# Kernel tuning notes

Hardware: AMD Instinct MI355X
Metric: run time of the kernel (lower is better)

The kernel has to match this reference:

```python
import jax, jax.numpy as jnp
import numpy as np

N_NODES = 100000
N_EDGES = 1600000


def _graphconv(h, src, dst, norm_src, norm_dst, W, b, n_nodes):
    # DGL GraphConv, norm='both': D_dst^{-1/2} * A * (D_src^{-1/2} * h) @ W + b, then relu
    h = h * norm_src[:, None]
    agg = jax.ops.segment_sum(h[src], dst, num_segments=n_nodes)  # [N, d] SpMM
    rst = agg @ W  # in_feats <= out_feats path: aggregate first, then W
    rst = rst * norm_dst[:, None]
    rst = rst + b
    return jax.nn.relu(rst)


def setup_inputs() -> dict:
    key = jax.random.key(0)
    ks = jax.random.split(key, 12)
    H = 64
    features = jax.random.normal(ks[0], (N_NODES, H), dtype=jnp.float32)
    src = jax.random.randint(ks[1], (N_EDGES,), 0, N_NODES, dtype=jnp.int64 if jax.config.jax_enable_x64 else jnp.int32)
    dst = jax.random.randint(ks[2], (N_EDGES,), 0, N_NODES, dtype=jnp.int64 if jax.config.jax_enable_x64 else jnp.int32)
    sc = 1.0 / np.sqrt(H)
    W1 = jax.random.normal(ks[3], (H, H), dtype=jnp.float32) * sc
    b1 = jnp.zeros((H,), dtype=jnp.float32)
    W2 = jax.random.normal(ks[4], (H, H), dtype=jnp.float32) * sc
    b2 = jnp.zeros((H,), dtype=jnp.float32)
    W3 = jax.random.normal(ks[5], (H, H), dtype=jnp.float32) * sc
    b3 = jnp.zeros((H,), dtype=jnp.float32)
    Wc = jax.random.normal(ks[6], (H, 10), dtype=jnp.float32) * sc
    bc = jnp.zeros((10,), dtype=jnp.float32)
    return {"features": features, "src": src, "dst": dst,
            "W1": W1, "b1": b1, "W2": W2, "b2": b2, "W3": W3, "b3": b3,
            "Wc": Wc, "bc": bc}


def reference(features, src, dst, W1, b1, W2, b2, W3, b3, Wc, bc):
    n = features.shape[0]
    ones = jnp.ones_like(src, dtype=features.dtype)
    deg_out = jax.ops.segment_sum(ones, src, num_segments=n)
    deg_in = jax.ops.segment_sum(ones, dst, num_segments=n)
    norm_src = jnp.clip(deg_out, 1.0) ** -0.5  # allow_zero_in_degree: clamp(min=1)
    norm_dst = jnp.clip(deg_in, 1.0) ** -0.5
    h = features
    for W, b in ((W1, b1), (W2, b2), (W3, b3)):
        # dropout p=0.0 / eval mode -> identity
        h = _graphconv(h, src, dst, norm_src, norm_dst, W, b, n)
    hg = jnp.mean(h, axis=0, keepdims=True)  # AvgPooling over the single graph -> [1, H]
    logits = hg @ Wc + bc  # [1, n_classes]
    return (logits, hg)
```

## Files before the change

kernel.cpp:

```cpp
#include <hip/hip_runtime.h>


__global__ void deg_kernel(const int* __restrict__ src, int* __restrict__ deg_out, int E) {
  int i = blockIdx.x * blockDim.x + threadIdx.x;
  if (i < E) atomicAdd(&deg_out[src[i]], 1);
}

__global__ void norm_kernel(const int* __restrict__ deg_out, float* __restrict__ ns, int N) {
  int i = blockIdx.x * blockDim.x + threadIdx.x;
  if (i < N) ns[i] = rsqrtf((float)max(deg_out[i], 1));
}

__global__ void fill_kernel(const int* __restrict__ src, const int* __restrict__ dst,
                            int* __restrict__ cursor, int* __restrict__ csr_src, int E) {
  int i = blockIdx.x * blockDim.x + threadIdx.x;
  if (i < E) {
    int d = dst[i];
    int p = atomicAdd(&cursor[d], 1);
    if (p < 64) csr_src[(size_t)d * 64 + p] = src[i];
  }
}

__device__ __forceinline__ ushort f32_to_bf16_rtne(float f) {
  uint u = __float_as_uint(f);
  uint r = (u + 0x7FFFu + ((u >> 16) & 1u)) >> 16;
  return (ushort)r;
}

__global__ __launch_bounds__(256) void gemm_scale_kernel(
    const float* __restrict__ h, const float* __restrict__ W,
    const float* __restrict__ ns, ushort* __restrict__ g, int N) {
  int lane = threadIdx.x & 63;
  int wave = (blockIdx.x << 2) + (threadIdx.x >> 6);
  int nwaves = gridDim.x << 2;
  float wcol[64];
#pragma unroll
  for (int k = 0; k < 64; k++) wcol[k] = W[k * 64 + lane];
  for (int n = wave; n < N; n += nwaves) {
    int nu = __builtin_amdgcn_readfirstlane(n);
    const float* __restrict__ hrow = h + (size_t)nu * 64;
    float acc = 0.f;
#pragma unroll
    for (int k = 0; k < 64; k++) acc = fmaf(hrow[k], wcol[k], acc);
    g[(size_t)nu * 64 + lane] = f32_to_bf16_rtne(acc * ns[nu]);
  }
}

__device__ __forceinline__ float bf16_load(const ushort* p) {
  return __uint_as_float((uint)(*p) << 16);
}

__global__ __launch_bounds__(256) void spmm_kernel(
    const ushort* __restrict__ g, const int* __restrict__ cnt,
    const int* __restrict__ csr_src, const float* __restrict__ bias,
    float* __restrict__ h_out, int N) {
  int lane = threadIdx.x & 63;
  int w = (blockIdx.x << 2) + (threadIdx.x >> 6);
  if (w >= N) return;
  int deg = cnt[w];
  const int* __restrict__ row = csr_src + (size_t)w * 64;
  int end = min(deg, 64);
  float scale = rsqrtf((float)max(deg, 1));
  float b = bias[lane];
  float acc = 0.f;
  int e = 0;
  for (; e + 8 <= end; e += 8) {
    int s0 = row[e + 0], s1 = row[e + 1], s2 = row[e + 2], s3 = row[e + 3];
    int s4 = row[e + 4], s5 = row[e + 5], s6 = row[e + 6], s7 = row[e + 7];
    float a0 = bf16_load(g + (size_t)s0 * 64 + lane);
    float a1 = bf16_load(g + (size_t)s1 * 64 + lane);
    float a2 = bf16_load(g + (size_t)s2 * 64 + lane);
    float a3 = bf16_load(g + (size_t)s3 * 64 + lane);
    float a4 = bf16_load(g + (size_t)s4 * 64 + lane);
    float a5 = bf16_load(g + (size_t)s5 * 64 + lane);
    float a6 = bf16_load(g + (size_t)s6 * 64 + lane);
    float a7 = bf16_load(g + (size_t)s7 * 64 + lane);
    acc += ((a0 + a1) + (a2 + a3)) + ((a4 + a5) + (a6 + a7));
  }
  for (; e + 2 <= end; e += 2) {
    int s0 = row[e + 0], s1 = row[e + 1];
    float a0 = bf16_load(g + (size_t)s0 * 64 + lane);
    float a1 = bf16_load(g + (size_t)s1 * 64 + lane);
    acc += a0 + a1;
  }
  if (e < end) acc += bf16_load(g + (size_t)row[e] * 64 + lane);
  float r = acc * scale + b;
  h_out[(size_t)w * 64 + lane] = fmaxf(r, 0.f);
}

__global__ __launch_bounds__(256) void pool_kernel(const float* __restrict__ h3,
                                                   float* __restrict__ pool, int N) {
  int lane = threadIdx.x & 63;
  int wid = threadIdx.x >> 6;
  float s = 0.f;
  for (int n = (blockIdx.x << 2) + wid; n < N; n += (gridDim.x << 2))
    s += h3[(size_t)n * 64 + lane];
  __shared__ float red[4][64];
  red[wid][lane] = s;
  __syncthreads();
  if (wid == 0) {
    float v = red[0][lane] + red[1][lane] + red[2][lane] + red[3][lane];
    atomicAdd(&pool[lane], v);
  }
}

__global__ void final_kernel(const float* __restrict__ pool, const float* __restrict__ Wc,
                             const float* __restrict__ bc, float* __restrict__ out, float invN) {
  int t = threadIdx.x;
  __shared__ float hg[64];
  float m = pool[t] * invN;
  hg[t] = m;
  out[10 + t] = m;
  __syncthreads();
  if (t < 10) {
    float s = bc[t];
#pragma unroll
    for (int k = 0; k < 64; k++) s = fmaf(hg[k], Wc[k * 10 + t], s);
    out[t] = s;
  }
}

extern "C" void kernel_launch(void* const* d_in, const int* in_sizes, int n_in,
                              void* d_out, int out_size, void* d_ws, size_t ws_size,
                              hipStream_t stream) {
  const float* features = (const float*)d_in[0];
  const int* src = (const int*)d_in[1];
  const int* dst = (const int*)d_in[2];
  const float* W1 = (const float*)d_in[3];
  const float* b1 = (const float*)d_in[4];
  const float* W2 = (const float*)d_in[5];
  const float* b2 = (const float*)d_in[6];
  const float* W3 = (const float*)d_in[7];
  const float* b3 = (const float*)d_in[8];
  const float* Wc = (const float*)d_in[9];
  const float* bc = (const float*)d_in[10];
  float* out = (float*)d_out;

  const int N = in_sizes[0] / 64;
  const int E = in_sizes[1];

  char* ws = (char*)d_ws;
  size_t off = 0;
  auto alloc = [&](size_t bytes) {
    void* p = ws + off;
    off = (off + bytes + 255) & ~(size_t)255;
    return p;
  };
  int* deg_out = (int*)alloc((size_t)N * 4);
  int* cursor = (int*)alloc((size_t)N * 4);
  float* pool = (float*)alloc(64 * 4);
  size_t zero_bytes = off;
  float* ns = (float*)alloc((size_t)N * 4);
  int* csr_src = (int*)alloc((size_t)N * 64 * 4);
  ushort* bufG = (ushort*)alloc((size_t)N * 64 * 2);
  float* bufH = (float*)alloc((size_t)N * 64 * 4);

  hipMemsetAsync(d_ws, 0, zero_bytes, stream);

  int eb = (E + 255) / 256;
  int nb = (N + 255) / 256;
  deg_kernel<<<eb, 256, 0, stream>>>(src, deg_out, E);
  norm_kernel<<<nb, 256, 0, stream>>>(deg_out, ns, N);
  fill_kernel<<<eb, 256, 0, stream>>>(src, dst, cursor, csr_src, E);

  int wb = (N + 3) / 4;

  gemm_scale_kernel<<<2048, 256, 0, stream>>>(features, W1, ns, bufG, N);
  spmm_kernel<<<wb, 256, 0, stream>>>(bufG, cursor, csr_src, b1, bufH, N);
  gemm_scale_kernel<<<2048, 256, 0, stream>>>(bufH, W2, ns, bufG, N);
  spmm_kernel<<<wb, 256, 0, stream>>>(bufG, cursor, csr_src, b2, bufH, N);
  gemm_scale_kernel<<<2048, 256, 0, stream>>>(bufH, W3, ns, bufG, N);
  spmm_kernel<<<wb, 256, 0, stream>>>(bufG, cursor, csr_src, b3, bufH, N);

  pool_kernel<<<256, 256, 0, stream>>>(bufH, pool, N);
  final_kernel<<<1, 64, 0, stream>>>(pool, Wc, bc, out, 1.0f / (float)N);
}
```

Measured before the change: 553.5 us.

## Fuse SpMM with next-layer GEMM, merge graph build kernels, fuse final SpMM with pooling

```diff
diff --git a/kernel.cpp b/kernel.cpp
--- a/kernel.cpp
+++ b/kernel.cpp
@@ -1,23 +1,16 @@
 #include <hip/hip_runtime.h>
 
 
-__global__ void deg_kernel(const int* __restrict__ src, int* __restrict__ deg_out, int E) {
-  int i = blockIdx.x * blockDim.x + threadIdx.x;
-  if (i < E) atomicAdd(&deg_out[src[i]], 1);
-}
-
-__global__ void norm_kernel(const int* __restrict__ deg_out, float* __restrict__ ns, int N) {
-  int i = blockIdx.x * blockDim.x + threadIdx.x;
-  if (i < N) ns[i] = rsqrtf((float)max(deg_out[i], 1));
-}
-
-__global__ void fill_kernel(const int* __restrict__ src, const int* __restrict__ dst,
-                            int* __restrict__ cursor, int* __restrict__ csr_src, int E) {
+__global__ void build_kernel(const int* __restrict__ src, const int* __restrict__ dst,
+                             int* __restrict__ deg_out, int* __restrict__ cursor,
+                             int* __restrict__ csr_src, int E) {
   int i = blockIdx.x * blockDim.x + threadIdx.x;
   if (i < E) {
+    int s = src[i];
     int d = dst[i];
+    atomicAdd(&deg_out[s], 1);
     int p = atomicAdd(&cursor[d], 1);
-    if (p < 64) csr_src[(size_t)d * 64 + p] = src[i];
+    if (p < 64) csr_src[(size_t)d * 64 + p] = s;
   }
 }
 
@@ -27,9 +20,13 @@
   return (ushort)r;
 }
 
-__global__ __launch_bounds__(256) void gemm_scale_kernel(
+__device__ __forceinline__ float bf16_load(const ushort* p) {
+  return __uint_as_float((uint)(*p) << 16);
+}
+
+__global__ __launch_bounds__(256) void gemm1_kernel(
     const float* __restrict__ h, const float* __restrict__ W,
-    const float* __restrict__ ns, ushort* __restrict__ g, int N) {
+    const int* __restrict__ deg_out, ushort* __restrict__ g, int N) {
   int lane = threadIdx.x & 63;
   int wave = (blockIdx.x << 2) + (threadIdx.x >> 6);
   int nwaves = gridDim.x << 2;
@@ -42,61 +39,96 @@
     float acc = 0.f;
 #pragma unroll
     for (int k = 0; k < 64; k++) acc = fmaf(hrow[k], wcol[k], acc);
-    g[(size_t)nu * 64 + lane] = f32_to_bf16_rtne(acc * ns[nu]);
+    float nsv = rsqrtf((float)max(deg_out[nu], 1));
+    g[(size_t)nu * 64 + lane] = f32_to_bf16_rtne(acc * nsv);
   }
 }
 
-__device__ __forceinline__ float bf16_load(const ushort* p) {
-  return __uint_as_float((uint)(*p) << 16);
+__global__ __launch_bounds__(256) void spmm_gemm_kernel(
+    const ushort* __restrict__ g_in, const int* __restrict__ cnt,
+    const int* __restrict__ csr_src, const int* __restrict__ deg_out,
+    const float* __restrict__ bias, const float* __restrict__ W,
+    ushort* __restrict__ g_out, int N) {
+  int lane = threadIdx.x & 63;
+  int wave = (blockIdx.x << 2) + (threadIdx.x >> 6);
+  int nwaves = gridDim.x << 2;
+  float wcol[64];
+#pragma unroll
+  for (int k = 0; k < 64; k++) wcol[k] = W[k * 64 + lane];
+  float b = bias[lane];
+  for (int w0 = wave; w0 < N; w0 += nwaves) {
+    int w = __builtin_amdgcn_readfirstlane(w0);
+    int deg = cnt[w];
+    const int* __restrict__ row = csr_src + (size_t)w * 64;
+    int end = min(deg, 64);
+    float acc = 0.f;
+    int e = 0;
+    for (; e + 8 <= end; e += 8) {
+      int s0 = row[e + 0], s1 = row[e + 1], s2 = row[e + 2], s3 = row[e + 3];
+      int s4 = row[e + 4], s5 = row[e + 5], s6 = row[e + 6], s7 = row[e + 7];
+      float a0 = bf16_load(g_in + (size_t)s0 * 64 + lane);
+      float a1 = bf16_load(g_in + (size_t)s1 * 64 + lane);
+      float a2 = bf16_load(g_in + (size_t)s2 * 64 + lane);
+      float a3 = bf16_load(g_in + (size_t)s3 * 64 + lane);
+      float a4 = bf16_load(g_in + (size_t)s4 * 64 + lane);
+      float a5 = bf16_load(g_in + (size_t)s5 * 64 + lane);
+      float a6 = bf16_load(g_in + (size_t)s6 * 64 + lane);
+      float a7 = bf16_load(g_in + (size_t)s7 * 64 + lane);
+      acc += ((a0 + a1) + (a2 + a3)) + ((a4 + a5) + (a6 + a7));
+    }
+    for (; e + 2 <= end; e += 2) {
+      int s0 = row[e + 0], s1 = row[e + 1];
+      acc += bf16_load(g_in + (size_t)s0 * 64 + lane) + bf16_load(g_in + (size_t)s1 * 64 + lane);
+    }
+    if (e < end) acc += bf16_load(g_in + (size_t)row[e] * 64 + lane);
+    float h = fmaxf(acc * rsqrtf((float)max(deg, 1)) + b, 0.f);
+    float o = 0.f;
+#pragma unroll
+    for (int k = 0; k < 64; k++) o = fmaf(__shfl(h, k, 64), wcol[k], o);
+    float nsv = rsqrtf((float)max(deg_out[w], 1));
+    g_out[(size_t)w * 64 + lane] = f32_to_bf16_rtne(o * nsv);
+  }
 }
 
-__global__ __launch_bounds__(256) void spmm_kernel(
-    const ushort* __restrict__ g, const int* __restrict__ cnt,
+__global__ __launch_bounds__(256) void spmm_pool_kernel(
+    const ushort* __restrict__ g_in, const int* __restrict__ cnt,
     const int* __restrict__ csr_src, const float* __restrict__ bias,
-    float* __restrict__ h_out, int N) {
-  int lane = threadIdx.x & 63;
-  int w = (blockIdx.x << 2) + (threadIdx.x >> 6);
-  if (w >= N) return;
-  int deg = cnt[w];
-  const int* __restrict__ row = csr_src + (size_t)w * 64;
-  int end = min(deg, 64);
-  float scale = rsqrtf((float)max(deg, 1));
-  float b = bias[lane];
-  float acc = 0.f;
-  int e = 0;
-  for (; e + 8 <= end; e += 8) {
-    int s0 = row[e + 0], s1 = row[e + 1], s2 = row[e + 2], s3 = row[e + 3];
-    int s4 = row[e + 4], s5 = row[e + 5], s6 = row[e + 6], s7 = row[e + 7];
-    float a0 = bf16_load(g + (size_t)s0 * 64 + lane);
-    float a1 = bf16_load(g + (size_t)s1 * 64 + lane);
-    float a2 = bf16_load(g + (size_t)s2 * 64 + lane);
-    float a3 = bf16_load(g + (size_t)s3 * 64 + lane);
-    float a4 = bf16_load(g + (size_t)s4 * 64 + lane);
-    float a5 = bf16_load(g + (size_t)s5 * 64 + lane);
-    float a6 = bf16_load(g + (size_t)s6 * 64 + lane);
-    float a7 = bf16_load(g + (size_t)s7 * 64 + lane);
-    acc += ((a0 + a1) + (a2 + a3)) + ((a4 + a5) + (a6 + a7));
-  }
-  for (; e + 2 <= end; e += 2) {
-    int s0 = row[e + 0], s1 = row[e + 1];
-    float a0 = bf16_load(g + (size_t)s0 * 64 + lane);
-    float a1 = bf16_load(g + (size_t)s1 * 64 + lane);
-    acc += a0 + a1;
-  }
-  if (e < end) acc += bf16_load(g + (size_t)row[e] * 64 + lane);
-  float r = acc * scale + b;
-  h_out[(size_t)w * 64 + lane] = fmaxf(r, 0.f);
-}
-
-__global__ __launch_bounds__(256) void pool_kernel(const float* __restrict__ h3,
-                                                   float* __restrict__ pool, int N) {
+    float* __restrict__ pool, int N) {
   int lane = threadIdx.x & 63;
   int wid = threadIdx.x >> 6;
-  float s = 0.f;
-  for (int n = (blockIdx.x << 2) + wid; n < N; n += (gridDim.x << 2))
-    s += h3[(size_t)n * 64 + lane];
+  int wave = (blockIdx.x << 2) + wid;
+  int nwaves = gridDim.x << 2;
+  float b = bias[lane];
+  float psum = 0.f;
+  for (int w0 = wave; w0 < N; w0 += nwaves) {
+    int w = __builtin_amdgcn_readfirstlane(w0);
+    int deg = cnt[w];
+    const int* __restrict__ row = csr_src + (size_t)w * 64;
+    int end = min(deg, 64);
+    float acc = 0.f;
+    int e = 0;
+    for (; e + 8 <= end; e += 8) {
+      int s0 = row[e + 0], s1 = row[e + 1], s2 = row[e + 2], s3 = row[e + 3];
+      int s4 = row[e + 4], s5 = row[e + 5], s6 = row[e + 6], s7 = row[e + 7];
+      float a0 = bf16_load(g_in + (size_t)s0 * 64 + lane);
+      float a1 = bf16_load(g_in + (size_t)s1 * 64 + lane);
+      float a2 = bf16_load(g_in + (size_t)s2 * 64 + lane);
+      float a3 = bf16_load(g_in + (size_t)s3 * 64 + lane);
+      float a4 = bf16_load(g_in + (size_t)s4 * 64 + lane);
+      float a5 = bf16_load(g_in + (size_t)s5 * 64 + lane);
+      float a6 = bf16_load(g_in + (size_t)s6 * 64 + lane);
+      float a7 = bf16_load(g_in + (size_t)s7 * 64 + lane);
+      acc += ((a0 + a1) + (a2 + a3)) + ((a4 + a5) + (a6 + a7));
+    }
+    for (; e + 2 <= end; e += 2) {
+      int s0 = row[e + 0], s1 = row[e + 1];
+      acc += bf16_load(g_in + (size_t)s0 * 64 + lane) + bf16_load(g_in + (size_t)s1 * 64 + lane);
+    }
+    if (e < end) acc += bf16_load(g_in + (size_t)row[e] * 64 + lane);
+    psum += fmaxf(acc * rsqrtf((float)max(deg, 1)) + b, 0.f);
+  }
   __shared__ float red[4][64];
-  red[wid][lane] = s;
+  red[wid][lane] = psum;
   __syncthreads();
   if (wid == 0) {
     float v = red[0][lane] + red[1][lane] + red[2][lane] + red[3][lane];
@@ -150,28 +182,18 @@
   int* cursor = (int*)alloc((size_t)N * 4);
   float* pool = (float*)alloc(64 * 4);
   size_t zero_bytes = off;
-  float* ns = (float*)alloc((size_t)N * 4);
   int* csr_src = (int*)alloc((size_t)N * 64 * 4);
-  ushort* bufG = (ushort*)alloc((size_t)N * 64 * 2);
-  float* bufH = (float*)alloc((size_t)N * 64 * 4);
+  ushort* bufG1 = (ushort*)alloc((size_t)N * 64 * 2);
+  ushort* bufG2 = (ushort*)alloc((size_t)N * 64 * 2);
 
   hipMemsetAsync(d_ws, 0, zero_bytes, stream);
 
   int eb = (E + 255) / 256;
-  int nb = (N + 255) / 256;
-  deg_kernel<<<eb, 256, 0, stream>>>(src, deg_out, E);
-  norm_kernel<<<nb, 256, 0, stream>>>(deg_out, ns, N);
-  fill_kernel<<<eb, 256, 0, stream>>>(src, dst, cursor, csr_src, E);
+  build_kernel<<<eb, 256, 0, stream>>>(src, dst, deg_out, cursor, csr_src, E);
 
-  int wb = (N + 3) / 4;
-
-  gemm_scale_kernel<<<2048, 256, 0, stream>>>(features, W1, ns, bufG, N);
-  spmm_kernel<<<wb, 256, 0, stream>>>(bufG, cursor, csr_src, b1, bufH, N);
-  gemm_scale_kernel<<<2048, 256, 0, stream>>>(bufH, W2, ns, bufG, N);
-  spmm_kernel<<<wb, 256, 0, stream>>>(bufG, cursor, csr_src, b2, bufH, N);
-  gemm_scale_kernel<<<2048, 256, 0, stream>>>(bufH, W3, ns, bufG, N);
-  spmm_kernel<<<wb, 256, 0, stream>>>(bufG, cursor, csr_src, b3, bufH, N);
-
-  pool_kernel<<<256, 256, 0, stream>>>(bufH, pool, N);
+  gemm1_kernel<<<2048, 256, 0, stream>>>(features, W1, deg_out, bufG1, N);
+  spmm_gemm_kernel<<<2048, 256, 0, stream>>>(bufG1, cursor, csr_src, deg_out, b1, W2, bufG2, N);
+  spmm_gemm_kernel<<<2048, 256, 0, stream>>>(bufG2, cursor, csr_src, deg_out, b2, W3, bufG1, N);
+  spmm_pool_kernel<<<2048, 256, 0, stream>>>(bufG1, cursor, csr_src, b3, pool, N);
   final_kernel<<<1, 64, 0, stream>>>(pool, Wc, bc, out, 1.0f / (float)N);
 }
```

After: 579.6 us. +4.7%, slower.

## Build CSR via two-pass bucket sort and fuse last SpMM with pooling

Applied to the files above, without the earlier changes.

```diff
diff --git a/kernel.cpp b/kernel.cpp
--- a/kernel.cpp
+++ b/kernel.cpp
@@ -1,24 +1,45 @@
 #include <hip/hip_runtime.h>
 
 
-__global__ void deg_kernel(const int* __restrict__ src, int* __restrict__ deg_out, int E) {
-  int i = blockIdx.x * blockDim.x + threadIdx.x;
-  if (i < E) atomicAdd(&deg_out[src[i]], 1);
-}
-
-__global__ void norm_kernel(const int* __restrict__ deg_out, float* __restrict__ ns, int N) {
-  int i = blockIdx.x * blockDim.x + threadIdx.x;
-  if (i < N) ns[i] = rsqrtf((float)max(deg_out[i], 1));
-}
-
-__global__ void fill_kernel(const int* __restrict__ src, const int* __restrict__ dst,
-                            int* __restrict__ cursor, int* __restrict__ csr_src, int E) {
+#define CAP 1536
+
+__global__ void bucketA_kernel(const int* __restrict__ src, const int* __restrict__ dst,
+                               int* __restrict__ deg_out, int* __restrict__ bcnt,
+                               uint* __restrict__ bbuf, int E) {
   int i = blockIdx.x * blockDim.x + threadIdx.x;
   if (i < E) {
+    int s = src[i];
     int d = dst[i];
-    int p = atomicAdd(&cursor[d], 1);
-    if (p < 64) csr_src[(size_t)d * 64 + p] = src[i];
-  }
+    atomicAdd(&deg_out[s], 1);
+    int b = d >> 6;
+    int pos = atomicAdd(&bcnt[b], 1);
+    if (pos < CAP) bbuf[(size_t)b * CAP + pos] = ((uint)s << 6) | (uint)(d & 63);
+  }
+}
+
+__global__ __launch_bounds__(256) void bucketB_kernel(const uint* __restrict__ bbuf,
+                                                      const int* __restrict__ bcnt,
+                                                      int* __restrict__ csr_src,
+                                                      int* __restrict__ deg_in, int N) {
+  __shared__ uint stage[64 * 64];
+  __shared__ int lcur[64];
+  int b = blockIdx.x;
+  int tid = threadIdx.x;
+  if (tid < 64) lcur[tid] = 0;
+  __syncthreads();
+  int cnt = min(bcnt[b], CAP);
+  const uint* __restrict__ bb = bbuf + (size_t)b * CAP;
+  for (int i = tid; i < cnt; i += 256) {
+    uint e = bb[i];
+    int dl = e & 63;
+    int p = atomicAdd(&lcur[dl], 1);
+    if (p < 64) stage[dl * 64 + p] = e >> 6;
+  }
+  __syncthreads();
+  int* __restrict__ outp = csr_src + (size_t)b * 4096;
+  for (int i = tid; i < 4096; i += 256) outp[i] = (int)stage[i];
+  int node = b * 64 + tid;
+  if (tid < 64 && node < N) deg_in[node] = min(lcur[tid], 64);
 }
 
 __device__ __forceinline__ ushort f32_to_bf16_rtne(float f) {
@@ -27,9 +48,13 @@
   return (ushort)r;
 }
 
+__device__ __forceinline__ float bf16_load(const ushort* p) {
+  return __uint_as_float((uint)(*p) << 16);
+}
+
 __global__ __launch_bounds__(256) void gemm_scale_kernel(
     const float* __restrict__ h, const float* __restrict__ W,
-    const float* __restrict__ ns, ushort* __restrict__ g, int N) {
+    const int* __restrict__ deg_out, ushort* __restrict__ g, int N) {
   int lane = threadIdx.x & 63;
   int wave = (blockIdx.x << 2) + (threadIdx.x >> 6);
   int nwaves = gridDim.x << 2;
@@ -42,61 +67,96 @@
     float acc = 0.f;
 #pragma unroll
     for (int k = 0; k < 64; k++) acc = fmaf(hrow[k], wcol[k], acc);
-    g[(size_t)nu * 64 + lane] = f32_to_bf16_rtne(acc * ns[nu]);
-  }
-}
-
-__device__ __forceinline__ float bf16_load(const ushort* p) {
-  return __uint_as_float((uint)(*p) << 16);
-}
+    float nsv = rsqrtf((float)max(deg_out[nu], 1));
+    g[(size_t)nu * 64 + lane] = f32_to_bf16_rtne(acc * nsv);
+  }
+}
+
+#define GATHER16(base)                                                   \
+  {                                                                      \
+    int s0 = row[e + 0], s1 = row[e + 1], s2 = row[e + 2], s3 = row[e + 3];   \
+    int s4 = row[e + 4], s5 = row[e + 5], s6 = row[e + 6], s7 = row[e + 7];   \
+    int s8 = row[e + 8], s9 = row[e + 9], sa = row[e + 10], sb = row[e + 11]; \
+    int sc = row[e + 12], sd = row[e + 13], se = row[e + 14], sf = row[e + 15];\
+    float a0 = bf16_load(base + (size_t)s0 * 64 + lane);                 \
+    float a1 = bf16_load(base + (size_t)s1 * 64 + lane);                 \
+    float a2 = bf16_load(base + (size_t)s2 * 64 + lane);                 \
+    float a3 = bf16_load(base + (size_t)s3 * 64 + lane);                 \
+    float a4 = bf16_load(base + (size_t)s4 * 64 + lane);                 \
+    float a5 = bf16_load(base + (size_t)s5 * 64 + lane);                 \
+    float a6 = bf16_load(base + (size_t)s6 * 64 + lane);                 \
+    float a7 = bf16_load(base + (size_t)s7 * 64 + lane);                 \
+    float a8 = bf16_load(base + (size_t)s8 * 64 + lane);                 \
+    float a9 = bf16_load(base + (size_t)s9 * 64 + lane);                 \
+    float aa = bf16_load(base + (size_t)sa * 64 + lane);                 \
+    float ab = bf16_load(base + (size_t)sb * 64 + lane);                 \
+    float ac = bf16_load(base + (size_t)sc * 64 + lane);                 \
+    float ad = bf16_load(base + (size_t)sd * 64 + lane);                 \
+    float ae = bf16_load(base + (size_t)se * 64 + lane);                 \
+    float af = bf16_load(base + (size_t)sf * 64 + lane);                 \
+    acc += (((a0 + a1) + (a2 + a3)) + ((a4 + a5) + (a6 + a7))) +         \
+           (((a8 + a9) + (aa + ab)) + ((ac + ad) + (ae + af)));          \
+  }
 
 __global__ __launch_bounds__(256) void spmm_kernel(
     const ushort* __restrict__ g, const int* __restrict__ cnt,
     const int* __restrict__ csr_src, const float* __restrict__ bias,
     float* __restrict__ h_out, int N) {
   int lane = threadIdx.x & 63;
-  int w = (blockIdx.x << 2) + (threadIdx.x >> 6);
-  if (w >= N) return;
+  int w0 = (blockIdx.x << 2) + (threadIdx.x >> 6);
+  if (w0 >= N) return;
+  int w = __builtin_amdgcn_readfirstlane(w0);
   int deg = cnt[w];
   const int* __restrict__ row = csr_src + (size_t)w * 64;
   int end = min(deg, 64);
-  float scale = rsqrtf((float)max(deg, 1));
   float b = bias[lane];
   float acc = 0.f;
   int e = 0;
-  for (; e + 8 <= end; e += 8) {
+  for (; e + 16 <= end; e += 16) GATHER16(g)
+  for (; e + 4 <= end; e += 4) {
     int s0 = row[e + 0], s1 = row[e + 1], s2 = row[e + 2], s3 = row[e + 3];
-    int s4 = row[e + 4], s5 = row[e + 5], s6 = row[e + 6], s7 = row[e + 7];
     float a0 = bf16_load(g + (size_t)s0 * 64 + lane);
     float a1 = bf16_load(g + (size_t)s1 * 64 + lane);
     float a2 = bf16_load(g + (size_t)s2 * 64 + lane);
     float a3 = bf16_load(g + (size_t)s3 * 64 + lane);
-    float a4 = bf16_load(g + (size_t)s4 * 64 + lane);
-    float a5 = bf16_load(g + (size_t)s5 * 64 + lane);
-    float a6 = bf16_load(g + (size_t)s6 * 64 + lane);
-    float a7 = bf16_load(g + (size_t)s7 * 64 + lane);
-    acc += ((a0 + a1) + (a2 + a3)) + ((a4 + a5) + (a6 + a7));
-  }
-  for (; e + 2 <= end; e += 2) {
-    int s0 = row[e + 0], s1 = row[e + 1];
-    float a0 = bf16_load(g + (size_t)s0 * 64 + lane);
-    float a1 = bf16_load(g + (size_t)s1 * 64 + lane);
-    acc += a0 + a1;
-  }
-  if (e < end) acc += bf16_load(g + (size_t)row[e] * 64 + lane);
-  float r = acc * scale + b;
+    acc += (a0 + a1) + (a2 + a3);
+  }
+  for (; e < end; e++) acc += bf16_load(g + (size_t)row[e] * 64 + lane);
+  float r = acc * rsqrtf((float)max(deg, 1)) + b;
   h_out[(size_t)w * 64 + lane] = fmaxf(r, 0.f);
 }
 
-__global__ __launch_bounds__(256) void pool_kernel(const float* __restrict__ h3,
-                                                   float* __restrict__ pool, int N) {
+__global__ __launch_bounds__(256) void spmm_pool_kernel(
+    const ushort* __restrict__ g, const int* __restrict__ cnt,
+    const int* __restrict__ csr_src, const float* __restrict__ bias,
+    float* __restrict__ pool, int N) {
   int lane = threadIdx.x & 63;
   int wid = threadIdx.x >> 6;
-  float s = 0.f;
-  for (int n = (blockIdx.x << 2) + wid; n < N; n += (gridDim.x << 2))
-    s += h3[(size_t)n * 64 + lane];
+  int wave = (blockIdx.x << 2) + wid;
+  int nwaves = gridDim.x << 2;
+  float b = bias[lane];
+  float psum = 0.f;
+  for (int w1 = wave; w1 < N; w1 += nwaves) {
+    int w = __builtin_amdgcn_readfirstlane(w1);
+    int deg = cnt[w];
+    const int* __restrict__ row = csr_src + (size_t)w * 64;
+    int end = min(deg, 64);
+    float acc = 0.f;
+    int e = 0;
+    for (; e + 16 <= end; e += 16) GATHER16(g)
+    for (; e + 4 <= end; e += 4) {
+      int s0 = row[e + 0], s1 = row[e + 1], s2 = row[e + 2], s3 = row[e + 3];
+      float a0 = bf16_load(g + (size_t)s0 * 64 + lane);
+      float a1 = bf16_load(g + (size_t)s1 * 64 + lane);
+      float a2 = bf16_load(g + (size_t)s2 * 64 + lane);
+      float a3 = bf16_load(g + (size_t)s3 * 64 + lane);
+      acc += (a0 + a1) + (a2 + a3);
+    }
+    for (; e < end; e++) acc += bf16_load(g + (size_t)row[e] * 64 + lane);
+    psum += fmaxf(acc * rsqrtf((float)max(deg, 1)) + b, 0.f);
+  }
   __shared__ float red[4][64];
-  red[wid][lane] = s;
+  red[wid][lane] = psum;
   __syncthreads();
   if (wid == 0) {
     float v = red[0][lane] + red[1][lane] + red[2][lane] + red[3][lane];
@@ -138,6 +198,7 @@
 
   const int N = in_sizes[0] / 64;
   const int E = in_sizes[1];
+  const int NB = (N + 63) >> 6;
 
   char* ws = (char*)d_ws;
   size_t off = 0;
@@ -147,31 +208,28 @@
     return p;
   };
   int* deg_out = (int*)alloc((size_t)N * 4);
-  int* cursor = (int*)alloc((size_t)N * 4);
+  int* bcnt = (int*)alloc((size_t)NB * 4);
   float* pool = (float*)alloc(64 * 4);
   size_t zero_bytes = off;
-  float* ns = (float*)alloc((size_t)N * 4);
-  int* csr_src = (int*)alloc((size_t)N * 64 * 4);
+  int* deg_in = (int*)alloc((size_t)N * 4);
+  uint* bbuf = (uint*)alloc((size_t)NB * CAP * 4);
+  int* csr_src = (int*)alloc((size_t)NB * 4096 * 4);
   ushort* bufG = (ushort*)alloc((size_t)N * 64 * 2);
   float* bufH = (float*)alloc((size_t)N * 64 * 4);
 
   hipMemsetAsync(d_ws, 0, zero_bytes, stream);
 
   int eb = (E + 255) / 256;
-  int nb = (N + 255) / 256;
-  deg_kernel<<<eb, 256, 0, stream>>>(src, deg_out, E);
-  norm_kernel<<<nb, 256, 0, stream>>>(deg_out, ns, N);
-  fill_kernel<<<eb, 256, 0, stream>>>(src, dst, cursor, csr_src, E);
+  bucketA_kernel<<<eb, 256, 0, stream>>>(src, dst, deg_out, bcnt, bbuf, E);
+  bucketB_kernel<<<NB, 256, 0, stream>>>(bbuf, bcnt, csr_src, deg_in, N);
 
   int wb = (N + 3) / 4;
 
-  gemm_scale_kernel<<<2048, 256, 0, stream>>>(features, W1, ns, bufG, N);
-  spmm_kernel<<<wb, 256, 0, stream>>>(bufG, cursor, csr_src, b1, bufH, N);
-  gemm_scale_kernel<<<2048, 256, 0, stream>>>(bufH, W2, ns, bufG, N);
-  spmm_kernel<<<wb, 256, 0, stream>>>(bufG, cursor, csr_src, b2, bufH, N);
-  gemm_scale_kernel<<<2048, 256, 0, stream>>>(bufH, W3, ns, bufG, N);
-  spmm_kernel<<<wb, 256, 0, stream>>>(bufG, cursor, csr_src, b3, bufH, N);
-
-  pool_kernel<<<256, 256, 0, stream>>>(bufH, pool, N);
+  gemm_scale_kernel<<<2048, 256, 0, stream>>>(features, W1, deg_out, bufG, N);
+  spmm_kernel<<<wb, 256, 0, stream>>>(bufG, deg_in, csr_src, b1, bufH, N);
+  gemm_scale_kernel<<<2048, 256, 0, stream>>>(bufH, W2, deg_out, bufG, N);
+  spmm_kernel<<<wb, 256, 0, stream>>>(bufG, deg_in, csr_src, b2, bufH, N);
+  gemm_scale_kernel<<<2048, 256, 0, stream>>>(bufH, W3, deg_out, bufG, N);
+  spmm_pool_kernel<<<2048, 256, 0, stream>>>(bufG, deg_in, csr_src, b3, pool, N);
   final_kernel<<<1, 64, 0, stream>>>(pool, Wc, bc, out, 1.0f / (float)N);
 }
```

After: 652.7 us. +17.9%, slower.

## Fuse graph build kernels, pair-edge bf16x2 gather, and fuse final SpMM with pooling

Applied to the files above, without the earlier changes.

```diff
diff --git a/kernel.cpp b/kernel.cpp
--- a/kernel.cpp
+++ b/kernel.cpp
@@ -1,23 +1,16 @@
 #include <hip/hip_runtime.h>
 
 
-__global__ void deg_kernel(const int* __restrict__ src, int* __restrict__ deg_out, int E) {
-  int i = blockIdx.x * blockDim.x + threadIdx.x;
-  if (i < E) atomicAdd(&deg_out[src[i]], 1);
-}
-
-__global__ void norm_kernel(const int* __restrict__ deg_out, float* __restrict__ ns, int N) {
-  int i = blockIdx.x * blockDim.x + threadIdx.x;
-  if (i < N) ns[i] = rsqrtf((float)max(deg_out[i], 1));
-}
-
-__global__ void fill_kernel(const int* __restrict__ src, const int* __restrict__ dst,
-                            int* __restrict__ cursor, int* __restrict__ csr_src, int E) {
+__global__ void build_kernel(const int* __restrict__ src, const int* __restrict__ dst,
+                             int* __restrict__ deg_out, int* __restrict__ cursor,
+                             int* __restrict__ csr_src, int E) {
   int i = blockIdx.x * blockDim.x + threadIdx.x;
   if (i < E) {
+    int s = src[i];
     int d = dst[i];
+    atomicAdd(&deg_out[s], 1);
     int p = atomicAdd(&cursor[d], 1);
-    if (p < 64) csr_src[(size_t)d * 64 + p] = src[i];
+    if (p < 64) csr_src[(size_t)d * 64 + p] = s;
   }
 }
 
@@ -29,7 +22,7 @@
 
 __global__ __launch_bounds__(256) void gemm_scale_kernel(
     const float* __restrict__ h, const float* __restrict__ W,
-    const float* __restrict__ ns, ushort* __restrict__ g, int N) {
+    const int* __restrict__ deg_out, ushort* __restrict__ g, int N) {
   int lane = threadIdx.x & 63;
   int wave = (blockIdx.x << 2) + (threadIdx.x >> 6);
   int nwaves = gridDim.x << 2;
@@ -42,65 +35,111 @@
     float acc = 0.f;
 #pragma unroll
     for (int k = 0; k < 64; k++) acc = fmaf(hrow[k], wcol[k], acc);
-    g[(size_t)nu * 64 + lane] = f32_to_bf16_rtne(acc * ns[nu]);
-  }
-}
-
-__device__ __forceinline__ float bf16_load(const ushort* p) {
-  return __uint_as_float((uint)(*p) << 16);
+    float nsv = rsqrtf((float)max(deg_out[nu], 1));
+    g[(size_t)nu * 64 + lane] = f32_to_bf16_rtne(acc * nsv);
+  }
+}
+
+__device__ __forceinline__ void gather_row(const uint* __restrict__ g32,
+                                           const int* __restrict__ row, int end,
+                                           int li, bool loHalf,
+                                           float& totLo, float& totHi) {
+  float accLo = 0.f, accHi = 0.f;
+  int e = 0;
+  for (; e + 16 <= end; e += 16) {
+    uint v[8];
+#pragma unroll
+    for (int p = 0; p < 8; p++) {
+      int sA = row[e + 2 * p];
+      int sB = row[e + 2 * p + 1];
+      int s = loHalf ? sA : sB;
+      v[p] = g32[(size_t)s * 32 + li];
+    }
+#pragma unroll
+    for (int p = 0; p < 8; p++) {
+      accLo += __uint_as_float(v[p] << 16);
+      accHi += __uint_as_float(v[p] & 0xFFFF0000u);
+    }
+  }
+  for (; e + 2 <= end; e += 2) {
+    int sA = row[e];
+    int sB = row[e + 1];
+    int s = loHalf ? sA : sB;
+    uint v = g32[(size_t)s * 32 + li];
+    accLo += __uint_as_float(v << 16);
+    accHi += __uint_as_float(v & 0xFFFF0000u);
+  }
+  if (e < end) {
+    int s = row[e];
+    uint v = 0u;
+    if (loHalf) v = g32[(size_t)s * 32 + li];
+    accLo += __uint_as_float(v << 16);
+    accHi += __uint_as_float(v & 0xFFFF0000u);
+  }
+  totLo = accLo + __shfl_xor(accLo, 32, 64);
+  totHi = accHi + __shfl_xor(accHi, 32, 64);
 }
 
 __global__ __launch_bounds__(256) void spmm_kernel(
     const ushort* __restrict__ g, const int* __restrict__ cnt,
     const int* __restrict__ csr_src, const float* __restrict__ bias,
     float* __restrict__ h_out, int N) {
+  const uint* __restrict__ g32 = (const uint*)g;
   int lane = threadIdx.x & 63;
-  int w = (blockIdx.x << 2) + (threadIdx.x >> 6);
-  if (w >= N) return;
+  int li = lane & 31;
+  bool loHalf = lane < 32;
+  int w0 = (blockIdx.x << 2) + (threadIdx.x >> 6);
+  if (w0 >= N) return;
+  int w = __builtin_amdgcn_readfirstlane(w0);
   int deg = cnt[w];
   const int* __restrict__ row = csr_src + (size_t)w * 64;
   int end = min(deg, 64);
+  float totLo, totHi;
+  gather_row(g32, row, end, li, loHalf, totLo, totHi);
   float scale = rsqrtf((float)max(deg, 1));
-  float b = bias[lane];
-  float acc = 0.f;
-  int e = 0;
-  for (; e + 8 <= end; e += 8) {
-    int s0 = row[e + 0], s1 = row[e + 1], s2 = row[e + 2], s3 = row[e + 3];
-    int s4 = row[e + 4], s5 = row[e + 5], s6 = row[e + 6], s7 = row[e + 7];
-    float a0 = bf16_load(g + (size_t)s0 * 64 + lane);
-    float a1 = bf16_load(g + (size_t)s1 * 64 + lane);
-    float a2 = bf16_load(g + (size_t)s2 * 64 + lane);
-    float a3 = bf16_load(g + (size_t)s3 * 64 + lane);
-    float a4 = bf16_load(g + (size_t)s4 * 64 + lane);
-    float a5 = bf16_load(g + (size_t)s5 * 64 + lane);
-    float a6 = bf16_load(g + (size_t)s6 * 64 + lane);
-    float a7 = bf16_load(g + (size_t)s7 * 64 + lane);
-    acc += ((a0 + a1) + (a2 + a3)) + ((a4 + a5) + (a6 + a7));
-  }
-  for (; e + 2 <= end; e += 2) {
-    int s0 = row[e + 0], s1 = row[e + 1];
-    float a0 = bf16_load(g + (size_t)s0 * 64 + lane);
-    float a1 = bf16_load(g + (size_t)s1 * 64 + lane);
-    acc += a0 + a1;
-  }
-  if (e < end) acc += bf16_load(g + (size_t)row[e] * 64 + lane);
-  float r = acc * scale + b;
-  h_out[(size_t)w * 64 + lane] = fmaxf(r, 0.f);
-}
-
-__global__ __launch_bounds__(256) void pool_kernel(const float* __restrict__ h3,
-                                                   float* __restrict__ pool, int N) {
+  if (loHalf) {
+    float2 r;
+    r.x = fmaxf(totLo * scale + bias[2 * li + 0], 0.f);
+    r.y = fmaxf(totHi * scale + bias[2 * li + 1], 0.f);
+    *(float2*)(h_out + (size_t)w * 64 + 2 * li) = r;
+  }
+}
+
+__global__ __launch_bounds__(256) void spmm_pool_kernel(
+    const ushort* __restrict__ g, const int* __restrict__ cnt,
+    const int* __restrict__ csr_src, const float* __restrict__ bias,
+    float* __restrict__ pool, int N) {
+  const uint* __restrict__ g32 = (const uint*)g;
   int lane = threadIdx.x & 63;
+  int li = lane & 31;
+  bool loHalf = lane < 32;
   int wid = threadIdx.x >> 6;
-  float s = 0.f;
-  for (int n = (blockIdx.x << 2) + wid; n < N; n += (gridDim.x << 2))
-    s += h3[(size_t)n * 64 + lane];
-  __shared__ float red[4][64];
-  red[wid][lane] = s;
+  int wave = (blockIdx.x << 2) + wid;
+  int nwaves = gridDim.x << 2;
+  float bLo = bias[2 * li + 0];
+  float bHi = bias[2 * li + 1];
+  float psumLo = 0.f, psumHi = 0.f;
+  for (int w1 = wave; w1 < N; w1 += nwaves) {
+    int w = __builtin_amdgcn_readfirstlane(w1);
+    int deg = cnt[w];
+    const int* __restrict__ row = csr_src + (size_t)w * 64;
+    int end = min(deg, 64);
+    float totLo, totHi;
+    gather_row(g32, row, end, li, loHalf, totLo, totHi);
+    float scale = rsqrtf((float)max(deg, 1));
+    psumLo += fmaxf(totLo * scale + bLo, 0.f);
+    psumHi += fmaxf(totHi * scale + bHi, 0.f);
+  }
+  __shared__ float redLo[4][64];
+  __shared__ float redHi[4][64];
+  redLo[wid][lane] = psumLo;
+  redHi[wid][lane] = psumHi;
   __syncthreads();
-  if (wid == 0) {
-    float v = red[0][lane] + red[1][lane] + red[2][lane] + red[3][lane];
-    atomicAdd(&pool[lane], v);
+  if (wid == 0 && loHalf) {
+    float vLo = redLo[0][lane] + redLo[1][lane] + redLo[2][lane] + redLo[3][lane];
+    float vHi = redHi[0][lane] + redHi[1][lane] + redHi[2][lane] + redHi[3][lane];
+    atomicAdd(&pool[2 * lane + 0], vLo);
+    atomicAdd(&pool[2 * lane + 1], vHi);
   }
 }
 
@@ -150,7 +189,6 @@
   int* cursor = (int*)alloc((size_t)N * 4);
   float* pool = (float*)alloc(64 * 4);
   size_t zero_bytes = off;
-  float* ns = (float*)alloc((size_t)N * 4);
   int* csr_src = (int*)alloc((size_t)N * 64 * 4);
   ushort* bufG = (ushort*)alloc((size_t)N * 64 * 2);
   float* bufH = (float*)alloc((size_t)N * 64 * 4);
@@ -158,20 +196,15 @@
   hipMemsetAsync(d_ws, 0, zero_bytes, stream);
 
   int eb = (E + 255) / 256;
-  int nb = (N + 255) / 256;
-  deg_kernel<<<eb, 256, 0, stream>>>(src, deg_out, E);
-  norm_kernel<<<nb, 256, 0, stream>>>(deg_out, ns, N);
-  fill_kernel<<<eb, 256, 0, stream>>>(src, dst, cursor, csr_src, E);
+  build_kernel<<<eb, 256, 0, stream>>>(src, dst, deg_out, cursor, csr_src, E);
 
   int wb = (N + 3) / 4;
 
-  gemm_scale_kernel<<<2048, 256, 0, stream>>>(features, W1, ns, bufG, N);
+  gemm_scale_kernel<<<2048, 256, 0, stream>>>(features, W1, deg_out, bufG, N);
   spmm_kernel<<<wb, 256, 0, stream>>>(bufG, cursor, csr_src, b1, bufH, N);
-  gemm_scale_kernel<<<2048, 256, 0, stream>>>(bufH, W2, ns, bufG, N);
+  gemm_scale_kernel<<<2048, 256, 0, stream>>>(bufH, W2, deg_out, bufG, N);
   spmm_kernel<<<wb, 256, 0, stream>>>(bufG, cursor, csr_src, b2, bufH, N);
-  gemm_scale_kernel<<<2048, 256, 0, stream>>>(bufH, W3, ns, bufG, N);
-  spmm_kernel<<<wb, 256, 0, stream>>>(bufG, cursor, csr_src, b3, bufH, N);
-
-  pool_kernel<<<256, 256, 0, stream>>>(bufH, pool, N);
+  gemm_scale_kernel<<<2048, 256, 0, stream>>>(bufH, W3, deg_out, bufG, N);
+  spmm_pool_kernel<<<2048, 256, 0, stream>>>(bufG, cursor, csr_src, b3, pool, N);
   final_kernel<<<1, 64, 0, stream>>>(pool, Wc, bc, out, 1.0f / (float)N);
 }
```

Measured after the change: 578.2 us. +4.5%, slower.
